# Performance work log

Hardware: AMD Instinct MI355X
Metric: run time of the kernel (lower is better)

Reference implementation:

```python
import jax, jax.numpy as jnp
import numpy as np

S, DM, H, DH, FF, L = 2048, 1024, 16, 64, 4096, 2
N_IMG, GH, GW = 4, 16, 32  # 4 images, each 16x32=512 tokens
THETA = 10000.0
LN_EPS = 1e-5


def _rope_tables():
    # 2D repeated rope: dim=DH, dim//4 freqs, x/y angles interleaved -> DH//2 per token
    fr = 1.0 / THETA ** (np.arange(0, DH, 4)[: DH // 4] / DH)  # [DH//4]
    pos = np.arange(GH * GW)
    xang = np.outer(pos % GW, fr)   # [512, DH//4]
    yang = np.outer(pos // GW, fr)  # [512, DH//4]
    ang = np.stack([xang, yang], axis=-1).reshape(GH * GW, DH // 2)  # [512, DH//2]
    ang = np.tile(ang, (N_IMG, 1))  # same grid repeated per image -> [S, DH//2]
    return np.cos(ang).astype(np.float32), np.sin(ang).astype(np.float32)


def setup_inputs() -> dict:
    key = jax.random.key(0)
    ks = jax.random.split(key, 8)
    scale = 0.02

    def rn(k, shape):
        return jax.random.normal(k, shape, jnp.float32) * scale

    x = jax.random.normal(ks[0], (S, DM), jnp.float32)
    input_row_offsets = jnp.array([0, 512, 1024, 1536, 2048], jnp.int32)
    cos_np, sin_np = _rope_tables()
    inp = {
        "x": x,
        "input_row_offsets": input_row_offsets,
        "freqs_cos": jnp.asarray(cos_np),
        "freqs_sin": jnp.asarray(sin_np),
        # stacked per-layer params [L, ...]; Linear weights stored as [in, out]
        "ln0_g": jnp.ones((L, DM), jnp.float32),
        "ln0_b": jnp.zeros((L, DM), jnp.float32),
        "ln1_g": jnp.ones((L, DM), jnp.float32),
        "ln1_b": jnp.zeros((L, DM), jnp.float32),
        "wqkv_w": rn(ks[1], (L, DM, 3 * DM)),
        "wqkv_b": jnp.zeros((L, 3 * DM), jnp.float32),
        "wo_w": rn(ks[2], (L, DM, DM)),
        "wo_b": jnp.zeros((L, DM), jnp.float32),
        "up_w": rn(ks[3], (L, DM, FF)),
        "up_b": jnp.zeros((L, FF), jnp.float32),
        "down_w": rn(ks[4], (L, FF, DM)),
        "down_b": jnp.zeros((L, DM), jnp.float32),
        "lnf_g": jnp.ones((DM,), jnp.float32),
        "lnf_b": jnp.zeros((DM,), jnp.float32),
    }
    return inp


def _layernorm(v, g, b):
    m = v.mean(-1, keepdims=True)
    var = v.var(-1, keepdims=True)
    return (v - m) * jax.lax.rsqrt(var + LN_EPS) * g + b


def _rope(t, cos, sin):
    # t: [S, H, DH]; pairs (even, odd) rotated by complex freqs (broadcast over heads)
    tr = t.reshape(S, H, DH // 2, 2)
    te, to = tr[..., 0], tr[..., 1]
    c = cos[:, None, :]
    s = sin[:, None, :]
    oe = te * c - to * s
    oo = te * s + to * c
    return jnp.stack([oe, oo], axis=-1).reshape(S, H, DH)


def reference(x, input_row_offsets, freqs_cos, freqs_sin,
              ln0_g, ln0_b, ln1_g, ln1_b, wqkv_w, wqkv_b, wo_w, wo_b,
              up_w, up_b, down_w, down_b, lnf_g, lnf_b):
    # Block-diagonal mask. NOTE: the torch reference ADDS the boolean mask
    # (True -> +1.0) to the logits, it does NOT mask with -inf. Replicated faithfully.
    seg = jnp.searchsorted(input_row_offsets, jnp.arange(S), side="right")
    maskf = (seg[:, None] == seg[None, :]).astype(jnp.float32)  # [S, S]
    inv_sqrt_d = 1.0 / jnp.sqrt(jnp.float32(DH))

    def layer(h, p):
        g0, b0, g1, b1, Wqkv, bqkv, Wo, bo, Wu, bu, Wd, bd = p
        y = _layernorm(h, g0, b0)
        qkv = (y @ Wqkv + bqkv).reshape(S, 3, H, DH)
        q, k, v = qkv[:, 0], qkv[:, 1], qkv[:, 2]
        q = _rope(q, freqs_cos, freqs_sin)
        k = _rope(k, freqs_cos, freqs_sin)
        aw = jnp.einsum("shd,thd->hst", q, k) * inv_sqrt_d + maskf[None]  # [H,S,S]
        aw = jax.nn.softmax(aw.astype(jnp.float32), axis=-1).astype(q.dtype)
        ao = jnp.einsum("hst,thd->shd", aw, v).reshape(S, DM)
        h = h + ao @ Wo + bo
        y = _layernorm(h, g1, b1)
        y = jax.nn.gelu(y @ Wu + bu, approximate=True)
        h = h + y @ Wd + bd
        return h, None

    params = (ln0_g, ln0_b, ln1_g, ln1_b, wqkv_w, wqkv_b, wo_w, wo_b,
              up_w, up_b, down_w, down_b)
    h, _ = jax.lax.scan(layer, x, params)
    return _layernorm(h, lnf_g, lnf_b)
```

## Files before the change

kernel.cpp:

```cpp
#include <hip/hip_runtime.h>
#include <hip/hip_bf16.h>
#include <stdint.h>
#include <math.h>

#define S_LEN 2048
#define DMODEL 1024
#define NHEAD 16
#define DHEAD 64
#define FFDIM 4096
#define NLAYER 2

using bf16 = __hip_bfloat16;
typedef __attribute__((ext_vector_type(8))) short bf16x8;
typedef __attribute__((ext_vector_type(4))) float f32x4;
typedef __attribute__((ext_vector_type(16))) float f32x16;
typedef __attribute__((ext_vector_type(4))) int i32x4;

#define MFMA16x16(A, B, C) __builtin_amdgcn_mfma_f32_16x16x32_bf16(A, B, C, 0, 0, 0)
#define MFMA32x32(A, B, C) __builtin_amdgcn_mfma_f32_32x32x16_bf16(A, B, C, 0, 0, 0)
#define EXP2(x) __builtin_amdgcn_exp2f(x)

__device__ __forceinline__ float bf2f(uint32_t u16bits) {
  union { uint32_t i; float f; } x;
  x.i = u16bits << 16;
  return x.f;
}
__device__ __forceinline__ uint16_t f2bf(float f) {
  return __builtin_bit_cast(uint16_t, __float2bfloat16(f));
}

__device__ __forceinline__ uint32_t cvtpk(float lo, float hi) {
  uint32_t r;
  asm("v_cvt_pk_bf16_f32 %0, %1, %2" : "=v"(r) : "v"(lo), "v"(hi));
  return r;
}
__device__ __forceinline__ void pl32swap(uint32_t& a, uint32_t& b) {
#if __has_builtin(__builtin_amdgcn_permlane32_swap)
  typedef __attribute__((ext_vector_type(2))) int i32x2;
  i32x2 r = __builtin_amdgcn_permlane32_swap((int)a, (int)b, false, false);
  a = (uint32_t)r.x;
  b = (uint32_t)r.y;
#else
  asm volatile("v_permlane32_swap_b32 %0, %1" : "+v"(a), "+v"(b));
#endif
}

__global__ __launch_bounds__(256) void k_tcast(const float* __restrict__ in,
                                               bf16* __restrict__ out,
                                               int R, int C) {
  __shared__ float tl[32][33];
  int t = threadIdx.x;
  int r0 = blockIdx.y * 32, c0 = blockIdx.x * 32;
  int cl = t & 31, rl = t >> 5;
#pragma unroll
  for (int i = 0; i < 4; ++i)
    tl[rl + i * 8][cl] = in[(size_t)(r0 + rl + i * 8) * C + c0 + cl];
  __syncthreads();
#pragma unroll
  for (int i = 0; i < 4; ++i)
    out[(size_t)(c0 + rl + i * 8) * R + r0 + cl] = __float2bfloat16(tl[cl][rl + i * 8]);
}

__device__ __forceinline__ void ln_store4(bf16* p, float a, float b, float c, float d) {
  uint2 u;
  u.x = (uint32_t)f2bf(a) | ((uint32_t)f2bf(b) << 16);
  u.y = (uint32_t)f2bf(c) | ((uint32_t)f2bf(d) << 16);
  *(uint2*)p = u;
}
__device__ __forceinline__ void ln_store4(float* p, float a, float b, float c, float d) {
  *(float4*)p = make_float4(a, b, c, d);
}

template <typename OUT>
__global__ __launch_bounds__(256) void k_ln(const float* __restrict__ h,
                                            const float* __restrict__ g,
                                            const float* __restrict__ b,
                                            OUT* __restrict__ y) {
  int row = blockIdx.x, t = threadIdx.x;
  const float4 v = ((const float4*)(h + (size_t)row * DMODEL))[t];
  float s = v.x + v.y + v.z + v.w;
  float s2 = v.x * v.x + v.y * v.y + v.z * v.z + v.w * v.w;
#pragma unroll
  for (int off = 32; off > 0; off >>= 1) {
    s += __shfl_down(s, off);
    s2 += __shfl_down(s2, off);
  }
  __shared__ float red[8];
  int w = t >> 6;
  if ((t & 63) == 0) { red[w] = s; red[4 + w] = s2; }
  __syncthreads();
  s = red[0] + red[1] + red[2] + red[3];
  s2 = red[4] + red[5] + red[6] + red[7];
  float mean = s * (1.0f / DMODEL);
  float var = s2 * (1.0f / DMODEL) - mean * mean;
  float rstd = rsqrtf(var + 1e-5f);
  float4 gv = ((const float4*)g)[t];
  float4 bv = ((const float4*)b)[t];
  float o0 = (v.x - mean) * rstd * gv.x + bv.x;
  float o1 = (v.y - mean) * rstd * gv.y + bv.y;
  float o2 = (v.z - mean) * rstd * gv.z + bv.z;
  float o3 = (v.w - mean) * rstd * gv.w + bv.w;
  ln_store4(y + (size_t)row * DMODEL + t * 4, o0, o1, o2, o3);
}

__global__ __launch_bounds__(256) void k_rope(const bf16* __restrict__ qkv,
                                              const float* __restrict__ fcos,
                                              const float* __restrict__ fsin,
                                              bf16* __restrict__ qr,
                                              bf16* __restrict__ kr) {
  int idx = blockIdx.x * 256 + threadIdx.x;
  int p = idx & 31;
  int hh = (idx >> 5) & (NHEAD - 1);
  int s = idx >> 9;
  float c = fcos[s * 32 + p], sn = fsin[s * 32 + p];
  int colq = hh * DHEAD + 2 * p;
  uint32_t rq = *(const uint32_t*)(qkv + (size_t)s * 3 * DMODEL + colq);
  uint32_t rk = *(const uint32_t*)(qkv + (size_t)s * 3 * DMODEL + DMODEL + colq);
  {
    float te = bf2f(rq & 0xffffu), to = bf2f(rq >> 16);
    uint32_t outv = (uint32_t)f2bf(te * c - to * sn) | ((uint32_t)f2bf(te * sn + to * c) << 16);
    *(uint32_t*)(qr + (size_t)s * DMODEL + colq) = outv;
  }
  {
    float te = bf2f(rk & 0xffffu), to = bf2f(rk >> 16);
    uint32_t outv = (uint32_t)f2bf(te * c - to * sn) | ((uint32_t)f2bf(te * sn + to * c) << 16);
    *(uint32_t*)(kr + (size_t)s * DMODEL + colq) = outv;
  }
}

__global__ __launch_bounds__(256) void k_tv(const bf16* __restrict__ qkv,
                                            bf16* __restrict__ vT) {
  __shared__ bf16 tl[64][65];
  int t = threadIdx.x;
  int hh = blockIdx.y;
  int sb = blockIdx.x * 64;
#pragma unroll
  for (int i = 0; i < 16; ++i) {
    int e = i * 256 + t;
    int sl = e >> 6, d = e & 63;
    tl[sl][d] = qkv[(size_t)(sb + sl) * 3 * DMODEL + 2 * DMODEL + hh * DHEAD + d];
  }
  __syncthreads();
#pragma unroll
  for (int i = 0; i < 16; ++i) {
    int e = i * 256 + t;
    int d = e >> 6, sl = e & 63;
    vT[(size_t)(hh * DHEAD + d) * S_LEN + sb + sl] = tl[sl][d];
  }
}

template <int EPI, int BM>
__global__ __launch_bounds__(256) void k_gemm2(const bf16* __restrict__ A,
                                               const bf16* __restrict__ BT,
                                               const float* __restrict__ bias,
                                               void* __restrict__ out,
                                               int M, int N, int K, int Kc) {
  constexpr int MF = BM / 32;
  __shared__ bf16 As[BM * 64];
  __shared__ bf16 Bs[128 * 64];
  int t = threadIdx.x;
  int w = t >> 6, l = t & 63, lr = l & 15, lg = l >> 4;
  int bm = blockIdx.x * BM, bn = blockIdx.y * 128;
  int k0 = blockIdx.z * Kc;
  int wm = (w >> 1) * (BM / 2), wn = (w & 1) * 64;

  f32x4 zero4 = {0.f, 0.f, 0.f, 0.f};
  f32x4 acc[MF][4];
#pragma unroll
  for (int mf = 0; mf < MF; ++mf)
#pragma unroll
    for (int nf = 0; nf < 4; ++nf) acc[mf][nf] = zero4;

  for (int kt = 0; kt < Kc; kt += 64) {
    __syncthreads();
#pragma unroll
    for (int i = 0; i < BM / 32; ++i) {
      int chunk = i * 256 + t;
      int row = chunk >> 3;
      int scol = ((chunk ^ row) & 7) << 3;
      __builtin_amdgcn_global_load_lds(
          (__attribute__((address_space(1))) void*)(A + (size_t)(bm + row) * K + k0 + kt + scol),
          (__attribute__((address_space(3))) void*)(As + chunk * 8), 16, 0, 0);
    }
#pragma unroll
    for (int i = 0; i < 4; ++i) {
      int chunk = i * 256 + t;
      int row = chunk >> 3;
      int scol = ((chunk ^ row) & 7) << 3;
      __builtin_amdgcn_global_load_lds(
          (__attribute__((address_space(1))) void*)(BT + (size_t)(bn + row) * K + k0 + kt + scol),
          (__attribute__((address_space(3))) void*)(Bs + chunk * 8), 16, 0, 0);
    }
    __syncthreads();
    bf16x8 af[2][MF], bfr[2][4];
#pragma unroll
    for (int h = 0; h < 2; ++h) {
#pragma unroll
      for (int mf = 0; mf < MF; ++mf) {
        int row = wm + mf * 16 + lr;
        af[h][mf] = *(const bf16x8*)(As + row * 64 + ((((h << 2) + lg) ^ (row & 7)) << 3));
      }
#pragma unroll
      for (int nf = 0; nf < 4; ++nf) {
        int row = wn + nf * 16 + lr;
        bfr[h][nf] = *(const bf16x8*)(Bs + row * 64 + ((((h << 2) + lg) ^ (row & 7)) << 3));
      }
    }
#pragma unroll
    for (int h = 0; h < 2; ++h)
#pragma unroll
      for (int mf = 0; mf < MF; ++mf)
#pragma unroll
        for (int nf = 0; nf < 4; ++nf)
          acc[mf][nf] = MFMA16x16(af[h][mf], bfr[h][nf], acc[mf][nf]);
  }

  if (EPI == 3) {
    float* outf = (float*)out + (size_t)blockIdx.z * ((size_t)M * N);
#pragma unroll
    for (int mf = 0; mf < MF; ++mf)
#pragma unroll
      for (int nf = 0; nf < 4; ++nf) {
        int col = bn + wn + nf * 16 + lr;
        int row0 = bm + wm + mf * 16 + lg * 4;
#pragma unroll
        for (int r = 0; r < 4; ++r)
          outf[(size_t)(row0 + r) * N + col] = acc[mf][nf][r];
      }
  } else {
    bf16* outb = (bf16*)out;
#pragma unroll
    for (int mf = 0; mf < MF; ++mf)
#pragma unroll
      for (int nf = 0; nf < 4; ++nf) {
        int col = bn + wn + nf * 16 + lr;
        float bv = bias[col];
        int row0 = bm + wm + mf * 16 + lg * 4;
#pragma unroll
        for (int r = 0; r < 4; ++r) {
          float v = acc[mf][nf][r] + bv;
          if (EPI == 2)
            v = 0.5f * v * (1.0f + tanhf(0.7978845608028654f * (v + 0.044715f * v * v * v)));
          outb[(size_t)(row0 + r) * N + col] = __float2bfloat16(v);
        }
      }
  }
}

template <int KS>
__global__ __launch_bounds__(256) void k_reduce(const float* __restrict__ part,
                                                const float* __restrict__ bias,
                                                float* __restrict__ hb,
                                                int MN, int N) {
  int i4 = (blockIdx.x * 256 + threadIdx.x) * 4;
  float4 r = *(const float4*)(hb + i4);
  float4 b = *(const float4*)(bias + (i4 & (N - 1)));
  float sx = r.x + b.x, sy = r.y + b.y, sz = r.z + b.z, sw = r.w + b.w;
#pragma unroll
  for (int ks = 0; ks < KS; ++ks) {
    float4 p = *(const float4*)(part + (size_t)ks * MN + i4);
    sx += p.x; sy += p.y; sz += p.z; sw += p.w;
  }
  *(float4*)(hb + i4) = make_float4(sx, sy, sz, sw);
}

__global__ __launch_bounds__(256, 4) void k_attn(const bf16* __restrict__ qr,
                                                 const bf16* __restrict__ kr,
                                                 const bf16* __restrict__ vT,
                                                 const int* __restrict__ offs,
                                                 bf16* __restrict__ ao) {
  __shared__ float oO[4][64][33];
  __shared__ float mM[4][32];
  __shared__ float lL[4][32];

  int t = threadIdx.x, w = t >> 6, l = t & 63;
  int ql = l & 31, hi = l >> 5, hi8 = hi * 8;
  int hh = blockIdx.x, qb = blockIdx.y * 32;
  int h64 = hh * DHEAD;

  constexpr float LOG2E = 1.4426950408889634f;
  constexpr float C1 = 0.125f * LOG2E;

  int q = qb + ql;
  int o0 = offs[0], o1 = offs[1], o2 = offs[2], o3 = offs[3], o4 = offs[4];
  int sl0 = -1073741824, sh0 = 1073741824;
  sl0 = (o0 <= q) ? o0 : sl0;
  sl0 = (o1 <= q) ? o1 : sl0;
  sl0 = (o2 <= q) ? o2 : sl0;
  sl0 = (o3 <= q) ? o3 : sl0;
  sl0 = (o4 <= q) ? o4 : sl0;
  sh0 = (o4 > q) ? o4 : sh0;
  sh0 = (o3 > q) ? o3 : sh0;
  sh0 = (o2 > q) ? o2 : sh0;
  sh0 = (o1 > q) ? o1 : sh0;
  sh0 = (o0 > q) ? o0 : sh0;
  uint32_t spanu = (uint32_t)(sh0 - sl0);

  const bf16* qbase = qr + (size_t)q * DMODEL + h64 + hi8;
  bf16x8 qf0 = *(const bf16x8*)(qbase);
  bf16x8 qf1 = *(const bf16x8*)(qbase + 16);
  bf16x8 qf2 = *(const bf16x8*)(qbase + 32);
  bf16x8 qf3 = *(const bf16x8*)(qbase + 48);

  f32x16 oC0, oC1;
#pragma unroll
  for (int r = 0; r < 16; ++r) { oC0[r] = 0.f; oC1[r] = 0.f; }
  float m_r = -1e30f, l_r = 0.f;

  const bf16* vrow = vT + (size_t)(h64 + ql) * S_LEN + hi8;

  for (int it = 0; it < 16; ++it) {
    int j0 = w * 512 + it * 32;
    const bf16* kbase = kr + (size_t)(j0 + ql) * DMODEL + h64 + hi8;
    bf16x8 kf0 = *(const bf16x8*)(kbase);
    bf16x8 kf1 = *(const bf16x8*)(kbase + 16);
    bf16x8 kf2 = *(const bf16x8*)(kbase + 32);
    bf16x8 kf3 = *(const bf16x8*)(kbase + 48);
    f32x16 sC;
#pragma unroll
    for (int r = 0; r < 16; ++r) sC[r] = 0.f;
    __builtin_amdgcn_s_setprio(1);
    sC = MFMA32x32(kf0, qf0, sC);
    sC = MFMA32x32(kf1, qf1, sC);
    sC = MFMA32x32(kf2, qf2, sC);
    sC = MFMA32x32(kf3, qf3, sC);
    __builtin_amdgcn_s_setprio(0);

    int tt = j0 + hi * 4 - sl0;
#pragma unroll
    for (int r = 0; r < 16; ++r) {
      int ku = tt + ((r & 3) + 8 * (r >> 2));
      float bias = ((uint32_t)ku < spanu) ? LOG2E : 0.0f;
      sC[r] = sC[r] * C1 + bias;
    }
    float rm = sC[0];
#pragma unroll
    for (int r = 1; r < 16; ++r) rm = fmaxf(rm, sC[r]);
    uint32_t ra = __builtin_bit_cast(uint32_t, rm), rb = ra;
    pl32swap(ra, rb);
    float rmax = fmaxf(__builtin_bit_cast(float, ra), __builtin_bit_cast(float, rb));

    if (__any(rmax > m_r + 8.0f)) {
      float mn = fmaxf(m_r, rmax);
      float fs = EXP2(m_r - mn);
      m_r = mn;
      l_r *= fs;
#pragma unroll
      for (int r = 0; r < 16; ++r) { oC0[r] *= fs; oC1[r] *= fs; }
    }
#pragma unroll
    for (int r = 0; r < 16; ++r) {
      float pv = EXP2(sC[r] - m_r);
      sC[r] = pv;
      l_r += pv;
    }
    uint32_t u0 = cvtpk(sC[0], sC[1]), u1 = cvtpk(sC[2], sC[3]);
    uint32_t u2 = cvtpk(sC[4], sC[5]), u3 = cvtpk(sC[6], sC[7]);
    uint32_t u4 = cvtpk(sC[8], sC[9]), u5 = cvtpk(sC[10], sC[11]);
    uint32_t u6 = cvtpk(sC[12], sC[13]), u7 = cvtpk(sC[14], sC[15]);
    pl32swap(u0, u2);
    pl32swap(u1, u3);
    pl32swap(u4, u6);
    pl32swap(u5, u7);
    i32x4 pi0 = {(int)u0, (int)u1, (int)u2, (int)u3};
    i32x4 pi1 = {(int)u4, (int)u5, (int)u6, (int)u7};
    bf16x8 pb0 = __builtin_bit_cast(bf16x8, pi0);
    bf16x8 pb1 = __builtin_bit_cast(bf16x8, pi1);

    const bf16* vbase = vrow + j0;
    bf16x8 va00 = *(const bf16x8*)(vbase);
    bf16x8 va01 = *(const bf16x8*)(vbase + 16);
    bf16x8 va10 = *(const bf16x8*)(vbase + 32 * S_LEN);
    bf16x8 va11 = *(const bf16x8*)(vbase + 32 * S_LEN + 16);
    __builtin_amdgcn_s_setprio(1);
    oC0 = MFMA32x32(va00, pb0, oC0);
    oC0 = MFMA32x32(va01, pb1, oC0);
    oC1 = MFMA32x32(va10, pb0, oC1);
    oC1 = MFMA32x32(va11, pb1, oC1);
    __builtin_amdgcn_s_setprio(0);
  }

  {
    uint32_t la = __builtin_bit_cast(uint32_t, l_r), lb = la;
    pl32swap(la, lb);
    l_r = __builtin_bit_cast(float, la) + __builtin_bit_cast(float, lb);
  }
  if (hi == 0) {
    mM[w][ql] = m_r;
    lL[w][ql] = l_r;
  }
#pragma unroll
  for (int r = 0; r < 16; ++r) {
    int d = (r & 3) + 8 * (r >> 2) + 4 * hi;
    oO[w][d][ql] = oC0[r];
    oO[w][d + 32][ql] = oC1[r];
  }
  __syncthreads();

  {
    int mq = t & 31, dbse = (t >> 5) * 8;
    float m0 = mM[0][mq], m1 = mM[1][mq], m2 = mM[2][mq], m3 = mM[3][mq];
    float ms = fmaxf(fmaxf(m0, m1), fmaxf(m2, m3));
    float a0 = EXP2(m0 - ms), a1 = EXP2(m1 - ms), a2 = EXP2(m2 - ms), a3 = EXP2(m3 - ms);
    float ll = a0 * lL[0][mq] + a1 * lL[1][mq] + a2 * lL[2][mq] + a3 * lL[3][mq];
    float inv = 1.0f / ll;
    uint4 pkv;
    uint32_t pw[4];
#pragma unroll
    for (int i = 0; i < 4; ++i) {
      int d0 = dbse + 2 * i, d1 = dbse + 2 * i + 1;
      float e0 = (a0 * oO[0][d0][mq] + a1 * oO[1][d0][mq] + a2 * oO[2][d0][mq] +
                  a3 * oO[3][d0][mq]) * inv;
      float e1 = (a0 * oO[0][d1][mq] + a1 * oO[1][d1][mq] + a2 * oO[2][d1][mq] +
                  a3 * oO[3][d1][mq]) * inv;
      pw[i] = (uint32_t)f2bf(e0) | ((uint32_t)f2bf(e1) << 16);
    }
    pkv.x = pw[0]; pkv.y = pw[1]; pkv.z = pw[2]; pkv.w = pw[3];
    *(uint4*)(ao + (size_t)(qb + mq) * DMODEL + h64 + dbse) = pkv;
  }
}

extern "C" void kernel_launch(void* const* d_in, const int* in_sizes, int n_in,
                              void* d_out, int out_size, void* d_ws, size_t ws_size,
                              hipStream_t stream) {
  const float* x = (const float*)d_in[0];
  const int* offs = (const int*)d_in[1];
  const float* fcos = (const float*)d_in[2];
  const float* fsin = (const float*)d_in[3];
  const float* ln0g = (const float*)d_in[4];
  const float* ln0b = (const float*)d_in[5];
  const float* ln1g = (const float*)d_in[6];
  const float* ln1b = (const float*)d_in[7];
  const float* wqkv = (const float*)d_in[8];
  const float* bqkv = (const float*)d_in[9];
  const float* wo = (const float*)d_in[10];
  const float* bo = (const float*)d_in[11];
  const float* wu = (const float*)d_in[12];
  const float* bu = (const float*)d_in[13];
  const float* wd = (const float*)d_in[14];
  const float* bd = (const float*)d_in[15];
  const float* lnfg = (const float*)d_in[16];
  const float* lnfb = (const float*)d_in[17];

  char* ws = (char*)d_ws;
  size_t off = 0;
  auto alloc = [&](size_t bytes) -> void* {
    void* p = ws + off;
    off += (bytes + 255) & ~(size_t)255;
    return p;
  };
  bf16* wqkvT = (bf16*)alloc((size_t)NLAYER * 3 * DMODEL * DMODEL * 2);
  bf16* woT = (bf16*)alloc((size_t)NLAYER * DMODEL * DMODEL * 2);
  bf16* wuT = (bf16*)alloc((size_t)NLAYER * DMODEL * FFDIM * 2);
  bf16* wdT = (bf16*)alloc((size_t)NLAYER * FFDIM * DMODEL * 2);
  float* hbuf = (float*)alloc((size_t)S_LEN * DMODEL * 4);
  bf16* ybuf = (bf16*)alloc((size_t)S_LEN * DMODEL * 2);
  bf16* qkv = (bf16*)alloc((size_t)S_LEN * 3 * DMODEL * 2);
  bf16* qrb = (bf16*)alloc((size_t)S_LEN * DMODEL * 2);
  bf16* krb = (bf16*)alloc((size_t)S_LEN * DMODEL * 2);
  bf16* vTb = (bf16*)alloc((size_t)S_LEN * DMODEL * 2);
  bf16* aob = (bf16*)alloc((size_t)S_LEN * DMODEL * 2);
  bf16* midb = (bf16*)alloc((size_t)S_LEN * FFDIM * 2);

  float* partWO = (float*)qkv;
  float* partDN = (float*)ybuf;

  for (int ly = 0; ly < NLAYER; ++ly) {
    k_tcast<<<dim3(3 * DMODEL / 32, DMODEL / 32), 256, 0, stream>>>(
        wqkv + (size_t)ly * DMODEL * 3 * DMODEL, wqkvT + (size_t)ly * 3 * DMODEL * DMODEL, DMODEL, 3 * DMODEL);
    k_tcast<<<dim3(DMODEL / 32, DMODEL / 32), 256, 0, stream>>>(
        wo + (size_t)ly * DMODEL * DMODEL, woT + (size_t)ly * DMODEL * DMODEL, DMODEL, DMODEL);
    k_tcast<<<dim3(FFDIM / 32, DMODEL / 32), 256, 0, stream>>>(
        wu + (size_t)ly * DMODEL * FFDIM, wuT + (size_t)ly * DMODEL * FFDIM, DMODEL, FFDIM);
    k_tcast<<<dim3(DMODEL / 32, FFDIM / 32), 256, 0, stream>>>(
        wd + (size_t)ly * FFDIM * DMODEL, wdT + (size_t)ly * FFDIM * DMODEL, FFDIM, DMODEL);
  }
  hipMemcpyAsync(hbuf, x, (size_t)S_LEN * DMODEL * 4, hipMemcpyDeviceToDevice, stream);

  for (int ly = 0; ly < NLAYER; ++ly) {
    k_ln<bf16><<<S_LEN, 256, 0, stream>>>(hbuf, ln0g + ly * DMODEL, ln0b + ly * DMODEL, ybuf);
    k_gemm2<0, 128><<<dim3(S_LEN / 128, 3 * DMODEL / 128, 1), 256, 0, stream>>>(
        ybuf, wqkvT + (size_t)ly * 3 * DMODEL * DMODEL, bqkv + ly * 3 * DMODEL, qkv,
        S_LEN, 3 * DMODEL, DMODEL, DMODEL);
    k_rope<<<S_LEN * NHEAD * 32 / 256, 256, 0, stream>>>(qkv, fcos, fsin, qrb, krb);
    k_tv<<<dim3(S_LEN / 64, NHEAD), 256, 0, stream>>>(qkv, vTb);
    k_attn<<<dim3(NHEAD, S_LEN / 32), 256, 0, stream>>>(qrb, krb, vTb, offs, aob);
    k_gemm2<3, 64><<<dim3(S_LEN / 64, DMODEL / 128, 2), 256, 0, stream>>>(
        aob, woT + (size_t)ly * DMODEL * DMODEL, nullptr, partWO,
        S_LEN, DMODEL, DMODEL, DMODEL / 2);
    k_reduce<2><<<S_LEN * DMODEL / 1024, 256, 0, stream>>>(
        partWO, bo + ly * DMODEL, hbuf, S_LEN * DMODEL, DMODEL);
    k_ln<bf16><<<S_LEN, 256, 0, stream>>>(hbuf, ln1g + ly * DMODEL, ln1b + ly * DMODEL, ybuf);
    k_gemm2<2, 128><<<dim3(S_LEN / 128, FFDIM / 128, 1), 256, 0, stream>>>(
        ybuf, wuT + (size_t)ly * DMODEL * FFDIM, bu + ly * FFDIM, midb,
        S_LEN, FFDIM, DMODEL, DMODEL);
    k_gemm2<3, 128><<<dim3(S_LEN / 128, DMODEL / 128, 4), 256, 0, stream>>>(
        midb, wdT + (size_t)ly * FFDIM * DMODEL, nullptr, partDN,
        S_LEN, DMODEL, FFDIM, FFDIM / 4);
    k_reduce<4><<<S_LEN * DMODEL / 1024, 256, 0, stream>>>(
        partDN, bd + ly * DMODEL, hbuf, S_LEN * DMODEL, DMODEL);
  }
  k_ln<float><<<S_LEN, 256, 0, stream>>>(hbuf, lnfg, lnfb, (float*)d_out);
}
```

Baseline: 420.4 us.

## Double-buffer GEMM LDS tiles with prefetch and swizzle block order

The GEMM kernel gets two LDS buffers for the A and B tiles. It issues the next K-tile's async global-to-LDS loads before computing on the current tile, which removes one barrier per iteration and overlaps memory with MFMA. It also remaps block indices in groups of 8 to improve cache locality. Doubled LDS use may reduce occupancy, and the remap assumes the grid size divides by 8.

```diff
diff --git a/kernel.cpp b/kernel.cpp
--- a/kernel.cpp
+++ b/kernel.cpp
@@ -156,11 +156,17 @@
                                                void* __restrict__ out,
                                                int M, int N, int K, int Kc) {
   constexpr int MF = BM / 32;
-  __shared__ bf16 As[BM * 64];
-  __shared__ bf16 Bs[128 * 64];
+  __shared__ bf16 As[2][BM * 64];
+  __shared__ bf16 Bs[2][128 * 64];
   int t = threadIdx.x;
   int w = t >> 6, l = t & 63, lr = l & 15, lg = l >> 4;
-  int bm = blockIdx.x * BM, bn = blockIdx.y * 128;
+
+  int nxy = gridDim.x * gridDim.y;
+  int bid = blockIdx.y * gridDim.x + blockIdx.x;
+  int chk8 = nxy >> 3;
+  int swz = (bid & 7) * chk8 + (bid >> 3);
+  int bx = swz % gridDim.x, by = swz / gridDim.x;
+  int bm = bx * BM, bn = by * 128;
   int k0 = blockIdx.z * Kc;
   int wm = (w >> 1) * (BM / 2), wn = (w & 1) * 64;
 
@@ -171,16 +177,15 @@
 #pragma unroll
     for (int nf = 0; nf < 4; ++nf) acc[mf][nf] = zero4;
 
-  for (int kt = 0; kt < Kc; kt += 64) {
-    __syncthreads();
+  auto stage = [&](int buf, int kk) {
 #pragma unroll
     for (int i = 0; i < BM / 32; ++i) {
       int chunk = i * 256 + t;
       int row = chunk >> 3;
       int scol = ((chunk ^ row) & 7) << 3;
       __builtin_amdgcn_global_load_lds(
-          (__attribute__((address_space(1))) void*)(A + (size_t)(bm + row) * K + k0 + kt + scol),
-          (__attribute__((address_space(3))) void*)(As + chunk * 8), 16, 0, 0);
+          (__attribute__((address_space(1))) void*)(A + (size_t)(bm + row) * K + kk + scol),
+          (__attribute__((address_space(3))) void*)(&As[buf][chunk * 8]), 16, 0, 0);
     }
 #pragma unroll
     for (int i = 0; i < 4; ++i) {
@@ -188,22 +193,29 @@
       int row = chunk >> 3;
       int scol = ((chunk ^ row) & 7) << 3;
       __builtin_amdgcn_global_load_lds(
-          (__attribute__((address_space(1))) void*)(BT + (size_t)(bn + row) * K + k0 + kt + scol),
-          (__attribute__((address_space(3))) void*)(Bs + chunk * 8), 16, 0, 0);
-    }
-    __syncthreads();
+          (__attribute__((address_space(1))) void*)(BT + (size_t)(bn + row) * K + kk + scol),
+          (__attribute__((address_space(3))) void*)(&Bs[buf][chunk * 8]), 16, 0, 0);
+    }
+  };
+
+  int nt = Kc / 64;
+  stage(0, k0);
+  __syncthreads();
+  int cur = 0;
+  for (int kt = 0; kt < nt; ++kt) {
+    if (kt + 1 < nt) stage(cur ^ 1, k0 + (kt + 1) * 64);
     bf16x8 af[2][MF], bfr[2][4];
 #pragma unroll
     for (int h = 0; h < 2; ++h) {
 #pragma unroll
       for (int mf = 0; mf < MF; ++mf) {
         int row = wm + mf * 16 + lr;
-        af[h][mf] = *(const bf16x8*)(As + row * 64 + ((((h << 2) + lg) ^ (row & 7)) << 3));
+        af[h][mf] = *(const bf16x8*)(&As[cur][row * 64 + ((((h << 2) + lg) ^ (row & 7)) << 3)]);
       }
 #pragma unroll
       for (int nf = 0; nf < 4; ++nf) {
         int row = wn + nf * 16 + lr;
-        bfr[h][nf] = *(const bf16x8*)(Bs + row * 64 + ((((h << 2) + lg) ^ (row & 7)) << 3));
+        bfr[h][nf] = *(const bf16x8*)(&Bs[cur][row * 64 + ((((h << 2) + lg) ^ (row & 7)) << 3)]);
       }
     }
 #pragma unroll
@@ -213,6 +225,8 @@
 #pragma unroll
         for (int nf = 0; nf < 4; ++nf)
           acc[mf][nf] = MFMA16x16(af[h][mf], bfr[h][nf], acc[mf][nf]);
+    __syncthreads();
+    cur ^= 1;
   }
 
   if (EPI == 3) {
```

Result: faster. 408.6 us (-2.8%).
